# Kernel optimization log

Hardware: AMD Instinct MI355X
Metric: run time of the kernel (lower is better)

The kernel has to match this reference:

```python
import jax, jax.numpy as jnp
import numpy as np
from jax import lax

STRIDES = (8, 16, 32, 64, 128)
LEVEL_HW = ((100, 128), (50, 64), (25, 32), (13, 16), (7, 8))
NUM_CLASSES = 80
PRE_NMS_THRESH = 0.05
PRE_NMS_TOPK = 1000
NMS_THRESH = 0.6
MAX_DET = 100
CLS_OFFSET = 1.0e4  # > max image coordinate, separates classes for joint NMS


def setup_inputs() -> dict:
    key = jax.random.key(0)
    B = 16
    ks = jax.random.split(key, 3 * len(LEVEL_HW))
    inp = {}
    i = 0
    for lvl, (h, w) in enumerate(LEVEL_HW):
        # shift logits down so sigmoid scores are mostly below the 0.05 candidate
        # threshold (realistic detection sparsity)
        inp[f"logits_p{lvl + 3}"] = jax.random.normal(ks[i], (B, NUM_CLASSES, h, w), jnp.float32) - 4.0; i += 1
        inp[f"bbox_p{lvl + 3}"] = jax.random.uniform(ks[i], (B, 4, h, w), jnp.float32, minval=0.0, maxval=64.0); i += 1
        inp[f"ctr_p{lvl + 3}"] = jax.random.normal(ks[i], (B, 1, h, w), jnp.float32); i += 1
    inp["im_info"] = jnp.tile(jnp.array([[800.0, 1024.0]], jnp.float32), (B, 1))
    return inp


def _locations(h, w, stride):
    # FCOSLocation: center of each stride cell -> [HW, 2] as (x, y)
    sx = jnp.arange(w, dtype=jnp.float32) * stride + stride // 2
    sy = jnp.arange(h, dtype=jnp.float32) * stride + stride // 2
    yy, xx = jnp.meshgrid(sy, sx, indexing="ij")
    return jnp.stack([xx.reshape(-1), yy.reshape(-1)], axis=-1)


def _nms_single(boxes, scores, classes):
    # boxes [K,4], scores [K] (descending), classes [K] int
    off = classes.astype(jnp.float32)[:, None] * CLS_OFFSET
    nb = boxes + off  # class-offset trick -> per-class NMS in one pass
    areas = jnp.maximum(nb[:, 2] - nb[:, 0], 0.0) * jnp.maximum(nb[:, 3] - nb[:, 1], 0.0)

    def body(sc, _):
        i = jnp.argmax(sc)
        s = sc[i]
        bi = nb[i]
        xx1 = jnp.maximum(bi[0], nb[:, 0])
        yy1 = jnp.maximum(bi[1], nb[:, 1])
        xx2 = jnp.minimum(bi[2], nb[:, 2])
        yy2 = jnp.minimum(bi[3], nb[:, 3])
        inter = jnp.maximum(xx2 - xx1, 0.0) * jnp.maximum(yy2 - yy1, 0.0)
        iou = inter / (areas[i] + areas - inter + 1e-9)
        sc2 = jnp.where(iou >= NMS_THRESH, -jnp.inf, sc).at[i].set(-jnp.inf)
        return sc2, (i, s > 0.0)

    _, (idxs, valid) = lax.scan(body, scores, None, length=MAX_DET)
    det = jnp.concatenate(
        [boxes[idxs], scores[idxs][:, None], classes[idxs].astype(jnp.float32)[:, None]],
        axis=-1,
    )  # [MAX_DET, 6] = x1,y1,x2,y2,score,class
    return jnp.where(valid[:, None], det, 0.0)


def _forward(logits_p3, bbox_p3, ctr_p3, logits_p4, bbox_p4, ctr_p4,
             logits_p5, bbox_p5, ctr_p5, logits_p6, bbox_p6, ctr_p6,
             logits_p7, bbox_p7, ctr_p7, im_info):
    levels = [(logits_p3, bbox_p3, ctr_p3), (logits_p4, bbox_p4, ctr_p4),
              (logits_p5, bbox_p5, ctr_p5), (logits_p6, bbox_p6, ctr_p6),
              (logits_p7, bbox_p7, ctr_p7)]
    scores_l, boxes_l = [], []
    for (lg, rg, ct), stride in zip(levels, STRIDES):
        B, C, H, W = lg.shape
        cls = jax.nn.sigmoid(lg).transpose(0, 2, 3, 1).reshape(B, H * W, C)
        cen = jax.nn.sigmoid(ct).transpose(0, 2, 3, 1).reshape(B, H * W, 1)
        # candidate threshold on raw class prob, then modulate by centerness
        comb = jnp.where(cls > PRE_NMS_THRESH, cls * cen, 0.0)
        locs = _locations(H, W, stride)  # [HW, 2]
        reg = rg.transpose(0, 2, 3, 1).reshape(B, H * W, 4)  # (l, t, r, b)
        bx = jnp.stack([locs[None, :, 0] - reg[..., 0],
                        locs[None, :, 1] - reg[..., 1],
                        locs[None, :, 0] + reg[..., 2],
                        locs[None, :, 1] + reg[..., 3]], axis=-1)
        scores_l.append(comb)
        boxes_l.append(bx)
    scores = jnp.concatenate(scores_l, axis=1)  # [B, N, C]
    boxes = jnp.concatenate(boxes_l, axis=1)    # [B, N, 4]
    B, N, C = scores.shape
    vals, idx = lax.top_k(scores.reshape(B, N * C), PRE_NMS_TOPK)  # [B, K]
    loc = idx // C
    cls_id = idx % C
    cand = jnp.take_along_axis(boxes, loc[..., None], axis=1)  # [B, K, 4]
    h = im_info[:, 0:1]
    w = im_info[:, 1:2]
    x1 = jnp.clip(cand[..., 0], 0.0, w - 1.0)
    y1 = jnp.clip(cand[..., 1], 0.0, h - 1.0)
    x2 = jnp.clip(cand[..., 2], 0.0, w - 1.0)
    y2 = jnp.clip(cand[..., 3], 0.0, h - 1.0)
    cand = jnp.stack([x1, y1, x2, y2], axis=-1)
    sc = jnp.where(vals > 0.0, jnp.sqrt(jnp.maximum(vals, 0.0) + 1e-12), 0.0)
    return jax.vmap(_nms_single)(cand, sc, cls_id)  # [B, MAX_DET, 6]


def reference(logits_p3, bbox_p3, ctr_p3, logits_p4, bbox_p4, ctr_p4,
              logits_p5, bbox_p5, ctr_p5, logits_p6, bbox_p6, ctr_p6,
              logits_p7, bbox_p7, ctr_p7, im_info):
    return _forward(logits_p3, bbox_p3, ctr_p3, logits_p4, bbox_p4, ctr_p4,
                    logits_p5, bbox_p5, ctr_p5, logits_p6, bbox_p6, ctr_p6,
                    logits_p7, bbox_p7, ctr_p7, im_info)
```

## Files before the change

### kernel.cpp

```cpp
#include <hip/hip_runtime.h>
#include <math.h>

#pragma clang fp contract(off)

#define NB 16
#define NC 80
#define NTOT 17064
#define TOPK 1000
#define NBINS 8192
#define CAP 4096
#define MAXDET 100
#define CNTSTRIDE 64
#define CHUNK 128
#define GH 128
#define WSEGCAP 256
#define FB 16

struct Ptrs {
    const float* lg[5];
    const float* bb[5];
    const float* ct[5];
};

__device__ __forceinline__ void level_of(int n, int& l, int& hw, int& W,
                                         int& stride, int& half, int& HW) {
    if (n < 12800)      { l = 0; hw = n;         W = 128; stride = 8;   half = 4;  HW = 12800; }
    else if (n < 16000) { l = 1; hw = n - 12800; W = 64;  stride = 16;  half = 8;  HW = 3200;  }
    else if (n < 16800) { l = 2; hw = n - 16000; W = 32;  stride = 32;  half = 16; HW = 800;   }
    else if (n < 17008) { l = 3; hw = n - 16800; W = 16;  stride = 64;  half = 32; HW = 208;   }
    else                { l = 4; hw = n - 17008; W = 8;   stride = 128; half = 64; HW = 56;    }
}

__device__ __forceinline__ float fast_sig(float x) {
    float e = __expf(-x);
    return __builtin_amdgcn_rcpf(1.0f + e);
}

#define HG_EMIT(BITS, NN, CC, POS)                                            \
    {                                                                         \
        int lb = (int)(((BITS) - 32u) >> 19) - BINBASE;                       \
        lb = (lb < 0) ? 0 : ((lb > 63) ? 63 : lb);                            \
        atomicAdd(&whv[lb], 1u);             \
        unsigned pos_ = (POS);                                                \
        if (pos_ < WSEGCAP) {                                                 \
            unsigned idx_ = (unsigned)((NN) * NC + (CC));                     \
            segw[pos_] = ((unsigned long long)(BITS) << 32) | idx_;           \
        }                                                                     \
    }

#define LOADLG(I, V)                                                          \
    V = make_float4(-40.f, -40.f, -40.f, -40.f);                              \
    if ((I) < NF4) V = *(const float4*)(lgb + (size_t)(I) * 4);

#define QGATE(I, V, FM, K0, K1, K2, K3, HWQ, CCQ)                             \
    unsigned FM = 0, K0 = 0, K1 = 0, K2 = 0, K3 = 0;                          \
    int HWQ = 0, CCQ = 0;                                                     \
    if ((V).x > -2.47f || (V).y > -2.47f || (V).z > -2.47f || (V).w > -2.47f) { \
        CCQ = (I) / HW4; HWQ = (I) - CCQ * HW4;                               \
        float4 cv = *(const float4*)(ctb + HWQ * 4);                          \
        K0 = __float_as_uint(fast_sig((V).x) * fast_sig(cv.x));               \
        K1 = __float_as_uint(fast_sig((V).y) * fast_sig(cv.y));               \
        K2 = __float_as_uint(fast_sig((V).z) * fast_sig(cv.z));               \
        K3 = __float_as_uint(fast_sig((V).w) * fast_sig(cv.w));               \
        FM = (K0 >= FB_LO ? 1u : 0u) | (K1 >= FB_LO ? 2u : 0u)                \
           | (K2 >= FB_LO ? 4u : 0u) | (K3 >= FB_LO ? 8u : 0u);               \
    }

template<int HW4, int NF4, int LVOFF>
__device__ __forceinline__ void histg_level(const float* lgb, const float* ctb,
        int tid, int bx, int gx, unsigned FB_LO, int BINBASE, unsigned* whv,
        unsigned& wcnt, unsigned long long* segw, unsigned long long ltmask) {
    const int stride = gx * 512;
    int i0 = bx * 512;
    if (i0 >= NF4) return;
    float4 va, vb;
    LOADLG(i0 + tid, va)
    LOADLG(i0 + 256 + tid, vb)
    for (; i0 < NF4; ) {
        int in0 = i0 + stride;
        int ia = i0 + tid, ib = i0 + 256 + tid;
        float4 nva, nvb;
        LOADLG(in0 + tid, nva)
        LOADLG(in0 + 256 + tid, nvb)
        QGATE(ia, va, fmA, kA0, kA1, kA2, kA3, hwa, cca)
        QGATE(ib, vb, fmB, kB0, kB1, kB2, kB3, hwb, ccb)
        unsigned long long m0 = __ballot(fmA & 1u), m1 = __ballot(fmA & 2u);
        unsigned long long m2 = __ballot(fmA & 4u), m3 = __ballot(fmA & 8u);
        unsigned long long m4 = __ballot(fmB & 1u), m5 = __ballot(fmB & 2u);
        unsigned long long m6 = __ballot(fmB & 4u), m7 = __ballot(fmB & 8u);
        if (m0 | m1 | m2 | m3 | m4 | m5 | m6 | m7) {
            unsigned t0 = (unsigned)__popcll(m0), t1 = (unsigned)__popcll(m1);
            unsigned t2 = (unsigned)__popcll(m2), t3 = (unsigned)__popcll(m3);
            unsigned t4 = (unsigned)__popcll(m4), t5 = (unsigned)__popcll(m5);
            unsigned t6 = (unsigned)__popcll(m6), t7 = (unsigned)__popcll(m7);
            unsigned wb = wcnt;
            wcnt = wb + t0 + t1 + t2 + t3 + t4 + t5 + t6 + t7;
            int nb0a = LVOFF + hwa * 4, nb0b = LVOFF + hwb * 4;
            if (fmA & 1u) HG_EMIT(kA0, nb0a + 0, cca, wb + (unsigned)__popcll(m0 & ltmask))
            if (fmA & 2u) HG_EMIT(kA1, nb0a + 1, cca, wb + t0 + (unsigned)__popcll(m1 & ltmask))
            if (fmA & 4u) HG_EMIT(kA2, nb0a + 2, cca, wb + t0 + t1 + (unsigned)__popcll(m2 & ltmask))
            if (fmA & 8u) HG_EMIT(kA3, nb0a + 3, cca, wb + t0 + t1 + t2 + (unsigned)__popcll(m3 & ltmask))
            if (fmB & 1u) HG_EMIT(kB0, nb0b + 0, ccb, wb + t0 + t1 + t2 + t3 + (unsigned)__popcll(m4 & ltmask))
            if (fmB & 2u) HG_EMIT(kB1, nb0b + 1, ccb, wb + t0 + t1 + t2 + t3 + t4 + (unsigned)__popcll(m5 & ltmask))
            if (fmB & 4u) HG_EMIT(kB2, nb0b + 2, ccb, wb + t0 + t1 + t2 + t3 + t4 + t5 + (unsigned)__popcll(m6 & ltmask))
            if (fmB & 8u) HG_EMIT(kB3, nb0b + 3, ccb, wb + t0 + t1 + t2 + t3 + t4 + t5 + t6 + (unsigned)__popcll(m7 & ltmask))
        }
        i0 = in0;
        va = nva; vb = nvb;
    }
}
#undef LOADLG
#undef QGATE
#undef HG_EMIT

__global__ void __launch_bounds__(256) k_histB(Ptrs p, unsigned* hist, unsigned* cnt2,
                                               unsigned* wavecnt, unsigned long long* segs) {
    __shared__ unsigned wh[4][64];
    int b = blockIdx.y, tid = threadIdx.x, bx = blockIdx.x, gx = gridDim.x;
    int wv = tid >> 6, lane = tid & 63;
    if (bx == 0 && tid == 0) cnt2[(size_t)b * CNTSTRIDE] = 0;
    ((unsigned*)wh)[tid] = 0;
    unsigned FB_LO = __float_as_uint(0.08f) - 64u;
    int BINBASE = (int)(__float_as_uint(0.08f) >> 19);
    unsigned* whv = wh[wv];
    unsigned long long ltmask = (1ULL << lane) - 1ULL;
    unsigned wcnt = 0;
    unsigned long long* segw = segs + (((size_t)b * GH + bx) * 4 + wv) * WSEGCAP;

    histg_level<3200, 256000,     0>(p.lg[0] + (size_t)b * NC * 12800, p.ct[0] + (size_t)b * 12800, tid, bx, gx, FB_LO, BINBASE, whv, wcnt, segw, ltmask);
    histg_level< 800,  64000, 12800>(p.lg[1] + (size_t)b * NC * 3200,  p.ct[1] + (size_t)b * 3200,  tid, bx, gx, FB_LO, BINBASE, whv, wcnt, segw, ltmask);
    histg_level< 200,  16000, 16000>(p.lg[2] + (size_t)b * NC * 800,   p.ct[2] + (size_t)b * 800,   tid, bx, gx, FB_LO, BINBASE, whv, wcnt, segw, ltmask);
    histg_level<  52,   4160, 16800>(p.lg[3] + (size_t)b * NC * 208,   p.ct[3] + (size_t)b * 208,   tid, bx, gx, FB_LO, BINBASE, whv, wcnt, segw, ltmask);
    histg_level<  14,   1120, 17008>(p.lg[4] + (size_t)b * NC * 56,    p.ct[4] + (size_t)b * 56,    tid, bx, gx, FB_LO, BINBASE, whv, wcnt, segw, ltmask);

    if (lane == 0)
        wavecnt[((size_t)b * GH + bx) * 4 + wv] = wcnt;
    __syncthreads();
    if (tid < 64) {
        unsigned s = wh[0][tid] + wh[1][tid] + wh[2][tid] + wh[3][tid];
        hist[((size_t)b * GH + bx) * 64 + tid] = s;
    }
}

template<int HW4, int NF4>
__device__ __forceinline__ void histf_level(const float* lgb, const float* ctb,
                                            int tid, unsigned* hist) {
    for (int i0 = 0; i0 < NF4; i0 += 256) {
        int i = i0 + tid;
        if (i < NF4) {
            int c = i / HW4, hwf = i - c * HW4;
            float4 v = *(const float4*)(lgb + c * (HW4 * 4) + hwf * 4);
            if (v.x > -2.95f || v.y > -2.95f || v.z > -2.95f || v.w > -2.95f) {
                float4 cv = *(const float4*)(ctb + hwf * 4);
                float xs[4] = {v.x, v.y, v.z, v.w};
                float cs[4] = {cv.x, cv.y, cv.z, cv.w};
#pragma unroll
                for (int j = 0; j < 4; ++j) {
                    float x = xs[j];
                    if (x > -2.95f) {
                        float cls = fast_sig(x);
                        if (cls > 0.04999f) {
                            bool in = true;
                            if (cls < 0.05001f)
                                in = (1.0f / (1.0f + expf(-x))) > 0.05f;
                            if (in) {
                                float cen = fast_sig(cs[j]);
                                unsigned bits = __float_as_uint(cls * cen);
                                unsigned cb = (bits > 32u) ? bits - 32u : 0u;
                                atomicAdd(&hist[cb >> 19], 1u);
                            }
                        }
                    }
                }
            }
        }
    }
}

#define CD_J(J, X, CT, NB0, CC, F, K)                                         \
    if ((X) > xpre) {                                                         \
        float cls = 1.0f / (1.0f + expf(-(X)));                               \
        if (cls > 0.05f) {                                                    \
            float cen = 1.0f / (1.0f + expf(-(CT)));                          \
            float comb = cls * cen;                                           \
            unsigned bits = __float_as_uint(comb);                            \
            if ((bits >> 19) >= Tb) {                                         \
                unsigned idx = (unsigned)(((NB0) + (J)) * NC + (CC));         \
                K = ((unsigned long long)bits << 32) | (0xFFFFFFFFu - idx);   \
                F = true;                                                     \
            }                                                                 \
        }                                                                     \
    }

template<int HW4, int NF4, int LVOFF>
__device__ __forceinline__ void compact_level(const float* lgb, const float* ctb,
        int tid, int lane, int bx, int gx, unsigned Tb, float xpre,
        unsigned* cntb, unsigned long long* selb, unsigned long long ltmask) {
    for (int i0 = bx * 512; i0 < NF4; i0 += gx * 512) {
        int ia = i0 + tid, ib2 = i0 + 256 + tid;
        bool la = ia < NF4, lb2 = ib2 < NF4;
        float4 va = make_float4(-9.f, -9.f, -9.f, -9.f);
        float4 vb = make_float4(-9.f, -9.f, -9.f, -9.f);
        int hwa = 0, hwb = 0, cca = 0, ccb = 0;
        if (la) {
            cca = ia / HW4; hwa = ia - cca * HW4;
            va = *(const float4*)(lgb + cca * (HW4 * 4) + hwa * 4);
        }
        if (lb2) {
            ccb = ib2 / HW4; hwb = ib2 - ccb * HW4;
            vb = *(const float4*)(lgb + ccb * (HW4 * 4) + hwb * 4);
        }
        {
            bool f0 = false, f1 = false, f2 = false, f3 = false;
            unsigned long long k0 = 0, k1 = 0, k2 = 0, k3 = 0;
            if (va.x > xpre || va.y > xpre || va.z > xpre || va.w > xpre) {
                float4 cv = *(const float4*)(ctb + hwa * 4);
                int nb0 = LVOFF + hwa * 4;
                CD_J(0, va.x, cv.x, nb0, cca, f0, k0)
                CD_J(1, va.y, cv.y, nb0, cca, f1, k1)
                CD_J(2, va.z, cv.z, nb0, cca, f2, k2)
                CD_J(3, va.w, cv.w, nb0, cca, f3, k3)
            }
            unsigned long long m0 = __ballot(f0), m1 = __ballot(f1);
            unsigned long long m2 = __ballot(f2), m3 = __ballot(f3);
            if (m0 | m1 | m2 | m3) {
                unsigned t0 = (unsigned)__popcll(m0), t1 = (unsigned)__popcll(m1);
                unsigned t2 = (unsigned)__popcll(m2), t3 = (unsigned)__popcll(m3);
                int basep = 0;
                if (lane == 0) basep = (int)atomicAdd(cntb, t0 + t1 + t2 + t3);
                basep = __shfl(basep, 0);
                if (f0) { int pos = basep + (int)__popcll(m0 & ltmask);                       if (pos < CAP) selb[pos] = k0; }
                if (f1) { int pos = basep + (int)t0 + (int)__popcll(m1 & ltmask);             if (pos < CAP) selb[pos] = k1; }
                if (f2) { int pos = basep + (int)(t0 + t1) + (int)__popcll(m2 & ltmask);      if (pos < CAP) selb[pos] = k2; }
                if (f3) { int pos = basep + (int)(t0 + t1 + t2) + (int)__popcll(m3 & ltmask); if (pos < CAP) selb[pos] = k3; }
            }
        }
        {
            bool f0 = false, f1 = false, f2 = false, f3 = false;
            unsigned long long k0 = 0, k1 = 0, k2 = 0, k3 = 0;
            if (vb.x > xpre || vb.y > xpre || vb.z > xpre || vb.w > xpre) {
                float4 cv = *(const float4*)(ctb + hwb * 4);
                int nb0 = LVOFF + hwb * 4;
                CD_J(0, vb.x, cv.x, nb0, ccb, f0, k0)
                CD_J(1, vb.y, cv.y, nb0, ccb, f1, k1)
                CD_J(2, vb.z, cv.z, nb0, ccb, f2, k2)
                CD_J(3, vb.w, cv.w, nb0, ccb, f3, k3)
            }
            unsigned long long m0 = __ballot(f0), m1 = __ballot(f1);
            unsigned long long m2 = __ballot(f2), m3 = __ballot(f3);
            if (m0 | m1 | m2 | m3) {
                unsigned t0 = (unsigned)__popcll(m0), t1 = (unsigned)__popcll(m1);
                unsigned t2 = (unsigned)__popcll(m2), t3 = (unsigned)__popcll(m3);
                int basep = 0;
                if (lane == 0) basep = (int)atomicAdd(cntb, t0 + t1 + t2 + t3);
                basep = __shfl(basep, 0);
                if (f0) { int pos = basep + (int)__popcll(m0 & ltmask);                       if (pos < CAP) selb[pos] = k0; }
                if (f1) { int pos = basep + (int)t0 + (int)__popcll(m1 & ltmask);             if (pos < CAP) selb[pos] = k1; }
                if (f2) { int pos = basep + (int)(t0 + t1) + (int)__popcll(m2 & ltmask);      if (pos < CAP) selb[pos] = k2; }
                if (f3) { int pos = basep + (int)(t0 + t1 + t2) + (int)__popcll(m3 & ltmask); if (pos < CAP) selb[pos] = k3; }
            }
        }
    }
}
#undef CD_J

__device__ __forceinline__ void run_compact(const Ptrs& p, int b, int tid, int lane,
        int bx, int gx, unsigned Tb, unsigned* cnt2, unsigned long long* sel) {
    float mthr = __uint_as_float(Tb << 19);
    float xpre = -2.95f;
    if (mthr > 1e-37f && mthr < 1.0f) {
        float lm = logf(mthr / (1.0f - mthr)) - 0.01f;
        if (lm > xpre) xpre = lm;
    }
    unsigned long long ltmask = (1ULL << lane) - 1ULL;
    unsigned* cntb = cnt2 + (size_t)b * CNTSTRIDE;
    unsigned long long* selb = sel + (size_t)b * CAP;
    compact_level<3200, 256000,     0>(p.lg[0] + (size_t)b * NC * 12800, p.ct[0] + (size_t)b * 12800, tid, lane, bx, gx, Tb, xpre, cntb, selb, ltmask);
    compact_level< 800,  64000, 12800>(p.lg[1] + (size_t)b * NC * 3200,  p.ct[1] + (size_t)b * 3200,  tid, lane, bx, gx, Tb, xpre, cntb, selb, ltmask);
    compact_level< 200,  16000, 16000>(p.lg[2] + (size_t)b * NC * 800,   p.ct[2] + (size_t)b * 800,   tid, lane, bx, gx, Tb, xpre, cntb, selb, ltmask);
    compact_level<  52,   4160, 16800>(p.lg[3] + (size_t)b * NC * 208,   p.ct[3] + (size_t)b * 208,   tid, lane, bx, gx, Tb, xpre, cntb, selb, ltmask);
    compact_level<  14,   1120, 17008>(p.lg[4] + (size_t)b * NC * 56,    p.ct[4] + (size_t)b * 56,    tid, lane, bx, gx, Tb, xpre, cntb, selb, ltmask);
}

__global__ void __launch_bounds__(256) k_filter(Ptrs p, const unsigned* hist,
        const unsigned* wavecnt, const unsigned long long* segs,
        unsigned* cnt2, unsigned long long* sel) {
    __shared__ unsigned part[4][64];
    __shared__ unsigned red[64];
    __shared__ unsigned fullh[NBINS];
    __shared__ int s_T, s_ok;
    __shared__ unsigned s_ovf;
    int b = blockIdx.y, tid = threadIdx.x, bx = blockIdx.x;
    int bin = tid & 63, grp = tid >> 6, lane = tid & 63, wv = tid >> 6;
    int BINBASE = (int)(__float_as_uint(0.08f) >> 19);

    unsigned s = 0;
    for (int blk = grp; blk < GH; blk += 4)
        s += hist[((size_t)b * GH + blk) * 64 + bin];
    part[grp][bin] = s;
    if (tid == 0) s_ovf = 0;
    __syncthreads();
    if (tid < 64) red[tid] = part[0][tid] + part[1][tid] + part[2][tid] + part[3][tid];
    unsigned ov = 0;
    for (int i = tid; i < GH * 4; i += 256)
        ov |= (wavecnt[(size_t)b * GH * 4 + i] > WSEGCAP) ? 1u : 0u;
    if (ov) atomicOr(&s_ovf, 1u);
    __syncthreads();
    if (tid == 0) {
        unsigned suf1 = 0;
        for (int i = 1; i < 64; ++i) suf1 += red[i];
        unsigned run = 0; int Tl = 0;
        for (int i = 63; i >= 1; --i) {
            run += red[i];
            if (run >= TOPK) { Tl = i; break; }
        }
        s_ok = (suf1 >= TOPK);
        s_T = Tl + BINBASE;
    }
    __syncthreads();

    if (s_ok && !s_ovf) {
        unsigned Tb = (unsigned)s_T;
        unsigned FLO = (Tb << 19) - 64u;
        unsigned* cntb = cnt2 + (size_t)b * CNTSTRIDE;
        unsigned long long* selb = sel + (size_t)b * CAP;
        unsigned long long ltmask = (1ULL << lane) - 1ULL;
        for (int sg = bx * 4 + wv; sg < GH * 4; sg += FB * 4) {
            unsigned cs = wavecnt[(size_t)b * GH * 4 + sg];
            if (cs > WSEGCAP) cs = WSEGCAP;
            const unsigned long long* sp = segs + ((size_t)b * GH * 4 + sg) * WSEGCAP;
            for (unsigned e0 = 0; e0 < cs; e0 += 64) {
                unsigned e = e0 + (unsigned)lane;
                bool take = false;
                unsigned long long key = 0;
                if (e < cs) {
                    unsigned long long kk = sp[e];
                    if ((unsigned)(kk >> 32) >= FLO) {
                        unsigned idx = (unsigned)kk;
                        int n = (int)(idx / NC), c = (int)(idx - (unsigned)n * NC);
                        int l, hw, W, stride, half, HW;
                        level_of(n, l, hw, W, stride, half, HW);
                        float x   = p.lg[l][(size_t)b * NC * HW + (size_t)c * HW + hw];
                        float ctv = p.ct[l][(size_t)b * HW + hw];
                        float cls = 1.0f / (1.0f + expf(-x));
                        if (cls > 0.05f) {
                            float cen = 1.0f / (1.0f + expf(-ctv));
                            unsigned bits = __float_as_uint(cls * cen);
                            if ((bits >> 19) >= Tb) {
                                key = ((unsigned long long)bits << 32) | (0xFFFFFFFFu - idx);
                                take = true;
                            }
                        }
                    }
                }
                unsigned long long m = __ballot(take);
                if (m) {
                    unsigned tot = (unsigned)__popcll(m);
                    int basep = 0;
                    if (lane == 0) basep = (int)atomicAdd(cntb, tot);
                    basep = __shfl(basep, 0);
                    if (take) {
                        int pos = basep + (int)__popcll(m & ltmask);
                        if (pos < CAP) selb[pos] = key;
                    }
                }
            }
        }
        return;
    }

    if (!s_ok) {
        if (bx != 0) return;
        for (int i = tid; i < NBINS; i += 256) fullh[i] = 0;
        __syncthreads();
        histf_level<3200, 256000>(p.lg[0] + (size_t)b * NC * 12800, p.ct[0] + (size_t)b * 12800, tid, fullh);
        histf_level< 800,  64000>(p.lg[1] + (size_t)b * NC * 3200,  p.ct[1] + (size_t)b * 3200,  tid, fullh);
        histf_level< 200,  16000>(p.lg[2] + (size_t)b * NC * 800,   p.ct[2] + (size_t)b * 800,   tid, fullh);
        histf_level<  52,   4160>(p.lg[3] + (size_t)b * NC * 208,   p.ct[3] + (size_t)b * 208,   tid, fullh);
        histf_level<  14,   1120>(p.lg[4] + (size_t)b * NC * 56,    p.ct[4] + (size_t)b * 56,    tid, fullh);
        __syncthreads();
        if (tid == 0) {
            unsigned run = 0; int Tf = 0;
            for (int i = NBINS - 1; i >= 0; --i) {
                run += fullh[i];
                if (run >= TOPK) { Tf = i; break; }
            }
            s_T = Tf;
        }
        __syncthreads();
        run_compact(p, b, tid, lane, 0, 1, (unsigned)s_T, cnt2, sel);
        return;
    }

    run_compact(p, b, tid, lane, bx, FB, (unsigned)s_T, cnt2, sel);
}

__global__ void __launch_bounds__(256) k_rankdec(Ptrs p, const unsigned* cnt,
                                                 const unsigned long long* sel,
                                                 const float* im_info, float* cand) {
    __shared__ __align__(16) unsigned long long keys[CAP];
    int b = blockIdx.y, tid = threadIdx.x;
    unsigned M = cnt[(size_t)b * CNTSTRIDE];
    if (M > CAP) M = CAP;
    int s0 = blockIdx.x * 256;
    if (s0 >= (int)M) return;
    int Mpad = (int)((M + 1u) & ~1u);
    for (int i = tid; i < Mpad; i += 256)
        keys[i] = (i < (int)M) ? sel[(size_t)b * CAP + i] : 0ULL;
    __syncthreads();

    int s = s0 + tid;
    if (s >= (int)M) return;
    unsigned long long k = keys[s];
    int rank = 0;
    for (int j = 0; j < Mpad; j += 2) {
        ulonglong2 kk = *(const ulonglong2*)&keys[j];
        rank += (kk.x > k) ? 1 : 0;
        rank += (kk.y > k) ? 1 : 0;
    }
    if (rank >= TOPK) return;

    float Him = im_info[b * 2 + 0], Wim = im_info[b * 2 + 1];
    float xmax = Wim - 1.0f, ymax = Him - 1.0f;
    unsigned sb = (unsigned)(k >> 32);
    unsigned idx = 0xFFFFFFFFu - (unsigned)(k & 0xFFFFFFFFu);
    float val = __uint_as_float(sb);
    int n = idx / NC, c = idx - n * NC;
    int l, hw, W, stride, half, HW;
    level_of(n, l, hw, W, stride, half, HW);
    int wx = hw % W, hy = hw / W;
    float locx = (float)(wx * stride + half);
    float locy = (float)(hy * stride + half);
    const float* bb = p.bb[l] + (size_t)b * 4 * HW + hw;
    float r0 = bb[0], r1 = bb[(size_t)HW], r2 = bb[(size_t)2 * HW], r3 = bb[(size_t)3 * HW];
    float x1 = locx - r0, y1 = locy - r1, x2 = locx + r2, y2 = locy + r3;
    x1 = fminf(fmaxf(x1, 0.f), xmax);
    y1 = fminf(fmaxf(y1, 0.f), ymax);
    x2 = fminf(fmaxf(x2, 0.f), xmax);
    y2 = fminf(fmaxf(y2, 0.f), ymax);
    float scv = sqrtf(val + 1e-12f);
    float off = (float)c * 10000.0f;
    float a0 = x1 + off, a1 = y1 + off, a2 = x2 + off, a3 = y2 + off;
    float area = fmaxf(a2 - a0, 0.f) * fmaxf(a3 - a1, 0.f);
    float* dst = cand + ((size_t)b * TOPK + rank) * 12;
    *(float4*)(dst + 0) = make_float4(x1, y1, x2, y2);
    *(float4*)(dst + 4) = make_float4(a0, a1, a2, a3);
    *(float4*)(dst + 8) = make_float4(area, scv, (float)c, 0.f);
}

__global__ void __launch_bounds__(64) k_nms(const unsigned* cnt, const float* cand,
                                            float* out) {
    __shared__ float4 s_ob[CHUNK], s_nb[CHUNK], s_ms[CHUNK];
    int b = blockIdx.x, lane = threadIdx.x;
    unsigned M = cnt[(size_t)b * CNTSTRIDE];
    if (M > CAP) M = CAP;
    int ncand = (int)M < TOPK ? (int)M : TOPK;
    const float* src = cand + (size_t)b * TOPK * 12;
    float* ob = out + (size_t)b * MAXDET * 6;

    int na = 0;
    float4 a0b = make_float4(0.f, 0.f, 0.f, 0.f);
    float4 a1b = make_float4(0.f, 0.f, 0.f, 0.f);
    float a0a = 0.f, a1a = 0.f;

    for (int base = 0; base < ncand && na < MAXDET; base += CHUNK) {
        int cn = ncand - base; if (cn > CHUNK) cn = CHUNK;
        for (int cidx = lane; cidx < cn; cidx += 64) {
            const float* s = src + (size_t)(base + cidx) * 12;
            s_ob[cidx] = *(const float4*)(s + 0);
            s_nb[cidx] = *(const float4*)(s + 4);
            s_ms[cidx] = *(const float4*)(s + 8);
        }
        __syncthreads();
        for (int r = 0; r < cn && na < MAXDET; ++r) {
            float4 cb = s_nb[r];
            float ca = s_ms[r].x;
            bool sup = false;
            if (lane < na) {
                float xx1 = fmaxf(a0b.x, cb.x);
                float yy1 = fmaxf(a0b.y, cb.y);
                float xx2 = fminf(a0b.z, cb.z);
                float yy2 = fminf(a0b.w, cb.w);
                float inter = fmaxf(xx2 - xx1, 0.f) * fmaxf(yy2 - yy1, 0.f);
                float iou = inter / (((a0a + ca) - inter) + 1e-9f);
                sup = (iou >= 0.6f);
            }
            if (lane + 64 < na) {
                float xx1 = fmaxf(a1b.x, cb.x);
                float yy1 = fmaxf(a1b.y, cb.y);
                float xx2 = fminf(a1b.z, cb.z);
                float yy2 = fminf(a1b.w, cb.w);
                float inter = fmaxf(xx2 - xx1, 0.f) * fmaxf(yy2 - yy1, 0.f);
                float iou = inter / (((a1a + ca) - inter) + 1e-9f);
                sup |= (iou >= 0.6f);
            }
            if (__ballot(sup) == 0ULL) {
                if (lane == (na & 63)) {
                    if (na < 64) { a0b = cb; a0a = ca; }
                    else         { a1b = cb; a1a = ca; }
                }
                if (lane == 0) {
                    float4 o4 = s_ob[r]; float4 m4 = s_ms[r];
                    ob[na * 6 + 0] = o4.x; ob[na * 6 + 1] = o4.y;
                    ob[na * 6 + 2] = o4.z; ob[na * 6 + 3] = o4.w;
                    ob[na * 6 + 4] = m4.y; ob[na * 6 + 5] = m4.z;
                }
                ++na;
            }
        }
        __syncthreads();
    }
    for (int q = na * 6 + lane; q < MAXDET * 6; q += 64)
        ob[q] = 0.f;
}

extern "C" void kernel_launch(void* const* d_in, const int* in_sizes, int n_in,
                              void* d_out, int out_size, void* d_ws, size_t ws_size,
                              hipStream_t stream) {
    Ptrs p;
    for (int l = 0; l < 5; ++l) {
        p.lg[l] = (const float*)d_in[3 * l + 0];
        p.bb[l] = (const float*)d_in[3 * l + 1];
        p.ct[l] = (const float*)d_in[3 * l + 2];
    }
    const float* im_info = (const float*)d_in[15];
    float* out = (float*)d_out;
    unsigned char* w = (unsigned char*)d_ws;

    unsigned* hist           = (unsigned*)(w);
    unsigned* cnt2           = (unsigned*)(w + 524288);
    unsigned* wavecnt        = (unsigned*)(w + 528384);
    unsigned long long* segs = (unsigned long long*)(w + 561152);
    unsigned long long* sel  = (unsigned long long*)(w + 17338368);
    float* cand              = (float*)(w + 17862656);

    k_histB<<<dim3(GH, NB), 256, 0, stream>>>(p, hist, cnt2, wavecnt, segs);
    k_filter<<<dim3(FB, NB), 256, 0, stream>>>(p, hist, wavecnt, segs, cnt2, sel);
    k_rankdec<<<dim3(16, NB), 256, 0, stream>>>(p, cnt2, sel, im_info, cand);
    k_nms<<<NB, 64, 0, stream>>>(cnt2, cand, out);
}
```

Baseline: 234.8 us.

## Split histogram pass into pure logit sweep plus separate gating kernel

The fused histogram kernel is split in two. A streaming sweep only thresholds raw logits and compacts survivors (raw value plus level-encoded index) per wave. A new small-grid gate kernel then loads centerness, computes the sigmoid product, builds the histogram and writes the filtered segments. The aim is to keep the bandwidth-bound sweep lean by taking the scattered centerness loads, transcendental math and shared-memory atomics off its critical path. The cost is an extra kernel launch, an extra round trip of survivors through global memory, and a larger workspace with new overflow caps.

```diff
diff --git a/kernel.cpp b/kernel.cpp
--- a/kernel.cpp
+++ b/kernel.cpp
@@ -13,7 +13,9 @@
 #define CNTSTRIDE 64
 #define CHUNK 128
 #define GH 128
-#define WSEGCAP 256
+#define ACAP 512
+#define HB 16
+#define BSEGCAP 2048
 #define FB 16
 
 struct Ptrs {
@@ -36,40 +38,22 @@
     return __builtin_amdgcn_rcpf(1.0f + e);
 }
 
-#define HG_EMIT(BITS, NN, CC, POS)                                            \
-    {                                                                         \
-        int lb = (int)(((BITS) - 32u) >> 19) - BINBASE;                       \
-        lb = (lb < 0) ? 0 : ((lb > 63) ? 63 : lb);                            \
-        atomicAdd(&whv[lb], 1u);             \
-        unsigned pos_ = (POS);                                                \
-        if (pos_ < WSEGCAP) {                                                 \
-            unsigned idx_ = (unsigned)((NN) * NC + (CC));                     \
-            segw[pos_] = ((unsigned long long)(BITS) << 32) | idx_;           \
-        }                                                                     \
-    }
-
 #define LOADLG(I, V)                                                          \
     V = make_float4(-40.f, -40.f, -40.f, -40.f);                              \
     if ((I) < NF4) V = *(const float4*)(lgb + (size_t)(I) * 4);
 
-#define QGATE(I, V, FM, K0, K1, K2, K3, HWQ, CCQ)                             \
-    unsigned FM = 0, K0 = 0, K1 = 0, K2 = 0, K3 = 0;                          \
-    int HWQ = 0, CCQ = 0;                                                     \
-    if ((V).x > -2.47f || (V).y > -2.47f || (V).z > -2.47f || (V).w > -2.47f) { \
-        CCQ = (I) / HW4; HWQ = (I) - CCQ * HW4;                               \
-        float4 cv = *(const float4*)(ctb + HWQ * 4);                          \
-        K0 = __float_as_uint(fast_sig((V).x) * fast_sig(cv.x));               \
-        K1 = __float_as_uint(fast_sig((V).y) * fast_sig(cv.y));               \
-        K2 = __float_as_uint(fast_sig((V).z) * fast_sig(cv.z));               \
-        K3 = __float_as_uint(fast_sig((V).w) * fast_sig(cv.w));               \
-        FM = (K0 >= FB_LO ? 1u : 0u) | (K1 >= FB_LO ? 2u : 0u)                \
-           | (K2 >= FB_LO ? 4u : 0u) | (K3 >= FB_LO ? 8u : 0u);               \
-    }
-
-template<int HW4, int NF4, int LVOFF>
-__device__ __forceinline__ void histg_level(const float* lgb, const float* ctb,
-        int tid, int bx, int gx, unsigned FB_LO, int BINBASE, unsigned* whv,
-        unsigned& wcnt, unsigned long long* segw, unsigned long long ltmask) {
+#define SW_EMIT(X, ENC, POS)                                                  \
+    {                                                                         \
+        unsigned pos_ = (POS);                                                \
+        if (pos_ < ACAP)                                                      \
+            survw[pos_] = ((unsigned long long)__float_as_uint(X) << 32)      \
+                        | (ENC);                                              \
+    }
+
+template<int NF4>
+__device__ __forceinline__ void sweepA(const float* lgb, unsigned lvl,
+        int tid, int bx, int gx, unsigned& wcnt,
+        unsigned long long* survw, unsigned long long ltmask) {
     const int stride = gx * 512;
     int i0 = bx * 512;
     if (i0 >= NF4) return;
@@ -82,12 +66,14 @@
         float4 nva, nvb;
         LOADLG(in0 + tid, nva)
         LOADLG(in0 + 256 + tid, nvb)
-        QGATE(ia, va, fmA, kA0, kA1, kA2, kA3, hwa, cca)
-        QGATE(ib, vb, fmB, kB0, kB1, kB2, kB3, hwb, ccb)
-        unsigned long long m0 = __ballot(fmA & 1u), m1 = __ballot(fmA & 2u);
-        unsigned long long m2 = __ballot(fmA & 4u), m3 = __ballot(fmA & 8u);
-        unsigned long long m4 = __ballot(fmB & 1u), m5 = __ballot(fmB & 2u);
-        unsigned long long m6 = __ballot(fmB & 4u), m7 = __ballot(fmB & 8u);
+        bool f0 = va.x > -2.47f, f1 = va.y > -2.47f;
+        bool f2 = va.z > -2.47f, f3 = va.w > -2.47f;
+        bool f4 = vb.x > -2.47f, f5 = vb.y > -2.47f;
+        bool f6 = vb.z > -2.47f, f7 = vb.w > -2.47f;
+        unsigned long long m0 = __ballot(f0), m1 = __ballot(f1);
+        unsigned long long m2 = __ballot(f2), m3 = __ballot(f3);
+        unsigned long long m4 = __ballot(f4), m5 = __ballot(f5);
+        unsigned long long m6 = __ballot(f6), m7 = __ballot(f7);
         if (m0 | m1 | m2 | m3 | m4 | m5 | m6 | m7) {
             unsigned t0 = (unsigned)__popcll(m0), t1 = (unsigned)__popcll(m1);
             unsigned t2 = (unsigned)__popcll(m2), t3 = (unsigned)__popcll(m3);
@@ -95,50 +81,110 @@
             unsigned t6 = (unsigned)__popcll(m6), t7 = (unsigned)__popcll(m7);
             unsigned wb = wcnt;
             wcnt = wb + t0 + t1 + t2 + t3 + t4 + t5 + t6 + t7;
-            int nb0a = LVOFF + hwa * 4, nb0b = LVOFF + hwb * 4;
-            if (fmA & 1u) HG_EMIT(kA0, nb0a + 0, cca, wb + (unsigned)__popcll(m0 & ltmask))
-            if (fmA & 2u) HG_EMIT(kA1, nb0a + 1, cca, wb + t0 + (unsigned)__popcll(m1 & ltmask))
-            if (fmA & 4u) HG_EMIT(kA2, nb0a + 2, cca, wb + t0 + t1 + (unsigned)__popcll(m2 & ltmask))
-            if (fmA & 8u) HG_EMIT(kA3, nb0a + 3, cca, wb + t0 + t1 + t2 + (unsigned)__popcll(m3 & ltmask))
-            if (fmB & 1u) HG_EMIT(kB0, nb0b + 0, ccb, wb + t0 + t1 + t2 + t3 + (unsigned)__popcll(m4 & ltmask))
-            if (fmB & 2u) HG_EMIT(kB1, nb0b + 1, ccb, wb + t0 + t1 + t2 + t3 + t4 + (unsigned)__popcll(m5 & ltmask))
-            if (fmB & 4u) HG_EMIT(kB2, nb0b + 2, ccb, wb + t0 + t1 + t2 + t3 + t4 + t5 + (unsigned)__popcll(m6 & ltmask))
-            if (fmB & 8u) HG_EMIT(kB3, nb0b + 3, ccb, wb + t0 + t1 + t2 + t3 + t4 + t5 + t6 + (unsigned)__popcll(m7 & ltmask))
+            unsigned ea = ((unsigned)ia << 2) | (lvl << 24);
+            unsigned eb = ((unsigned)ib << 2) | (lvl << 24);
+            if (f0) SW_EMIT(va.x, ea + 0u, wb + (unsigned)__popcll(m0 & ltmask))
+            if (f1) SW_EMIT(va.y, ea + 1u, wb + t0 + (unsigned)__popcll(m1 & ltmask))
+            if (f2) SW_EMIT(va.z, ea + 2u, wb + t0 + t1 + (unsigned)__popcll(m2 & ltmask))
+            if (f3) SW_EMIT(va.w, ea + 3u, wb + t0 + t1 + t2 + (unsigned)__popcll(m3 & ltmask))
+            if (f4) SW_EMIT(vb.x, eb + 0u, wb + t0 + t1 + t2 + t3 + (unsigned)__popcll(m4 & ltmask))
+            if (f5) SW_EMIT(vb.y, eb + 1u, wb + t0 + t1 + t2 + t3 + t4 + (unsigned)__popcll(m5 & ltmask))
+            if (f6) SW_EMIT(vb.z, eb + 2u, wb + t0 + t1 + t2 + t3 + t4 + t5 + (unsigned)__popcll(m6 & ltmask))
+            if (f7) SW_EMIT(vb.w, eb + 3u, wb + t0 + t1 + t2 + t3 + t4 + t5 + t6 + (unsigned)__popcll(m7 & ltmask))
         }
         i0 = in0;
         va = nva; vb = nvb;
     }
 }
 #undef LOADLG
-#undef QGATE
-#undef HG_EMIT
-
-__global__ void __launch_bounds__(256) k_histB(Ptrs p, unsigned* hist, unsigned* cnt2,
-                                               unsigned* wavecnt, unsigned long long* segs) {
-    __shared__ unsigned wh[4][64];
+#undef SW_EMIT
+
+__global__ void __launch_bounds__(256) k_sweep(Ptrs p, unsigned* cnt2,
+        unsigned* survwcnt, unsigned long long* surv) {
     int b = blockIdx.y, tid = threadIdx.x, bx = blockIdx.x, gx = gridDim.x;
     int wv = tid >> 6, lane = tid & 63;
     if (bx == 0 && tid == 0) cnt2[(size_t)b * CNTSTRIDE] = 0;
+    unsigned long long ltmask = (1ULL << lane) - 1ULL;
+    unsigned wcnt = 0;
+    unsigned long long* survw = surv + (((size_t)b * GH + bx) * 4 + wv) * ACAP;
+
+    sweepA<256000>(p.lg[0] + (size_t)b * NC * 12800, 0u, tid, bx, gx, wcnt, survw, ltmask);
+    sweepA< 64000>(p.lg[1] + (size_t)b * NC * 3200,  1u, tid, bx, gx, wcnt, survw, ltmask);
+    sweepA< 16000>(p.lg[2] + (size_t)b * NC * 800,   2u, tid, bx, gx, wcnt, survw, ltmask);
+    sweepA<  4160>(p.lg[3] + (size_t)b * NC * 208,   3u, tid, bx, gx, wcnt, survw, ltmask);
+    sweepA<  1120>(p.lg[4] + (size_t)b * NC * 56,    4u, tid, bx, gx, wcnt, survw, ltmask);
+
+    if (lane == 0)
+        survwcnt[((size_t)b * GH + bx) * 4 + wv] = wcnt;
+}
+
+__global__ void __launch_bounds__(256) k_gate(Ptrs p, const unsigned* survwcnt,
+        const unsigned long long* surv, unsigned* hist, unsigned* wavecnt,
+        unsigned long long* segs) {
+    __shared__ unsigned wh[4][64];
+    int b = blockIdx.y, tid = threadIdx.x, bx = blockIdx.x;
+    int wv = tid >> 6, lane = tid & 63;
     ((unsigned*)wh)[tid] = 0;
     unsigned FB_LO = __float_as_uint(0.08f) - 64u;
     int BINBASE = (int)(__float_as_uint(0.08f) >> 19);
     unsigned* whv = wh[wv];
     unsigned long long ltmask = (1ULL << lane) - 1ULL;
     unsigned wcnt = 0;
-    unsigned long long* segw = segs + (((size_t)b * GH + bx) * 4 + wv) * WSEGCAP;
-
-    histg_level<3200, 256000,     0>(p.lg[0] + (size_t)b * NC * 12800, p.ct[0] + (size_t)b * 12800, tid, bx, gx, FB_LO, BINBASE, whv, wcnt, segw, ltmask);
-    histg_level< 800,  64000, 12800>(p.lg[1] + (size_t)b * NC * 3200,  p.ct[1] + (size_t)b * 3200,  tid, bx, gx, FB_LO, BINBASE, whv, wcnt, segw, ltmask);
-    histg_level< 200,  16000, 16000>(p.lg[2] + (size_t)b * NC * 800,   p.ct[2] + (size_t)b * 800,   tid, bx, gx, FB_LO, BINBASE, whv, wcnt, segw, ltmask);
-    histg_level<  52,   4160, 16800>(p.lg[3] + (size_t)b * NC * 208,   p.ct[3] + (size_t)b * 208,   tid, bx, gx, FB_LO, BINBASE, whv, wcnt, segw, ltmask);
-    histg_level<  14,   1120, 17008>(p.lg[4] + (size_t)b * NC * 56,    p.ct[4] + (size_t)b * 56,    tid, bx, gx, FB_LO, BINBASE, whv, wcnt, segw, ltmask);
-
+    unsigned long long* segw = segs + (((size_t)b * HB + bx) * 4 + wv) * BSEGCAP;
+
+    for (int sg = bx * 4 + wv; sg < GH * 4; sg += HB * 4) {
+        unsigned cs = survwcnt[(size_t)b * GH * 4 + sg];
+        if (cs > ACAP) cs = ACAP;
+        const unsigned long long* sp = surv + ((size_t)b * GH * 4 + sg) * ACAP;
+        for (unsigned e0 = 0; e0 < cs; e0 += 64) {
+            unsigned e = e0 + (unsigned)lane;
+            bool take = false;
+            unsigned bits = 0, idx = 0;
+            if (e < cs) {
+                unsigned long long kk = sp[e];
+                float x = __uint_as_float((unsigned)(kk >> 32));
+                unsigned enc = (unsigned)kk;
+                int lvl = (int)(enc >> 24);
+                int e4 = (int)(enc & 0x00FFFFFFu);
+                int HW, NOFF;
+                const float* ctb;
+                if (lvl == 0)      { HW = 12800; NOFF = 0;     ctb = p.ct[0]; }
+                else if (lvl == 1) { HW = 3200;  NOFF = 12800; ctb = p.ct[1]; }
+                else if (lvl == 2) { HW = 800;   NOFF = 16000; ctb = p.ct[2]; }
+                else if (lvl == 3) { HW = 208;   NOFF = 16800; ctb = p.ct[3]; }
+                else               { HW = 56;    NOFF = 17008; ctb = p.ct[4]; }
+                int cc = e4 / HW;
+                int hwl = e4 - cc * HW;
+                float ctv = ctb[(size_t)b * HW + hwl];
+                unsigned b2 = __float_as_uint(fast_sig(x) * fast_sig(ctv));
+                if (b2 >= FB_LO) {
+                    int lb = (int)((b2 - 32u) >> 19) - BINBASE;
+                    lb = (lb < 0) ? 0 : ((lb > 63) ? 63 : lb);
+                    atomicAdd(&whv[lb], 1u);
+                    bits = b2;
+                    idx = (unsigned)((NOFF + hwl) * NC + cc);
+                    take = true;
+                }
+            }
+            unsigned long long m = __ballot(take);
+            if (m) {
+                unsigned tot = (unsigned)__popcll(m);
+                unsigned wb = wcnt;
+                wcnt = wb + tot;
+                if (take) {
+                    unsigned pos = wb + (unsigned)__popcll(m & ltmask);
+                    if (pos < BSEGCAP)
+                        segw[pos] = ((unsigned long long)bits << 32) | idx;
+                }
+            }
+        }
+    }
     if (lane == 0)
-        wavecnt[((size_t)b * GH + bx) * 4 + wv] = wcnt;
+        wavecnt[((size_t)b * HB + bx) * 4 + wv] = wcnt;
     __syncthreads();
     if (tid < 64) {
         unsigned s = wh[0][tid] + wh[1][tid] + wh[2][tid] + wh[3][tid];
-        hist[((size_t)b * GH + bx) * 64 + tid] = s;
+        hist[((size_t)b * HB + bx) * 64 + tid] = s;
     }
 }
 
@@ -283,8 +329,8 @@
 }
 
 __global__ void __launch_bounds__(256) k_filter(Ptrs p, const unsigned* hist,
-        const unsigned* wavecnt, const unsigned long long* segs,
-        unsigned* cnt2, unsigned long long* sel) {
+        const unsigned* survwcnt, const unsigned* wavecnt,
+        const unsigned long long* segs, unsigned* cnt2, unsigned long long* sel) {
     __shared__ unsigned part[4][64];
     __shared__ unsigned red[64];
     __shared__ unsigned fullh[NBINS];
@@ -295,15 +341,17 @@
     int BINBASE = (int)(__float_as_uint(0.08f) >> 19);
 
     unsigned s = 0;
-    for (int blk = grp; blk < GH; blk += 4)
-        s += hist[((size_t)b * GH + blk) * 64 + bin];
+    for (int blk = grp; blk < HB; blk += 4)
+        s += hist[((size_t)b * HB + blk) * 64 + bin];
     part[grp][bin] = s;
     if (tid == 0) s_ovf = 0;
     __syncthreads();
     if (tid < 64) red[tid] = part[0][tid] + part[1][tid] + part[2][tid] + part[3][tid];
     unsigned ov = 0;
     for (int i = tid; i < GH * 4; i += 256)
-        ov |= (wavecnt[(size_t)b * GH * 4 + i] > WSEGCAP) ? 1u : 0u;
+        ov |= (survwcnt[(size_t)b * GH * 4 + i] > ACAP) ? 1u : 0u;
+    for (int i = tid; i < HB * 4; i += 256)
+        ov |= (wavecnt[(size_t)b * HB * 4 + i] > BSEGCAP) ? 1u : 0u;
     if (ov) atomicOr(&s_ovf, 1u);
     __syncthreads();
     if (tid == 0) {
@@ -325,10 +373,10 @@
         unsigned* cntb = cnt2 + (size_t)b * CNTSTRIDE;
         unsigned long long* selb = sel + (size_t)b * CAP;
         unsigned long long ltmask = (1ULL << lane) - 1ULL;
-        for (int sg = bx * 4 + wv; sg < GH * 4; sg += FB * 4) {
-            unsigned cs = wavecnt[(size_t)b * GH * 4 + sg];
-            if (cs > WSEGCAP) cs = WSEGCAP;
-            const unsigned long long* sp = segs + ((size_t)b * GH * 4 + sg) * WSEGCAP;
+        for (int sg = bx * 4 + wv; sg < HB * 4; sg += FB * 4) {
+            unsigned cs = wavecnt[(size_t)b * HB * 4 + sg];
+            if (cs > BSEGCAP) cs = BSEGCAP;
+            const unsigned long long* sp = segs + ((size_t)b * HB * 4 + sg) * BSEGCAP;
             for (unsigned e0 = 0; e0 < cs; e0 += 64) {
                 unsigned e = e0 + (unsigned)lane;
                 bool take = false;
@@ -528,14 +576,17 @@
     unsigned char* w = (unsigned char*)d_ws;
 
     unsigned* hist           = (unsigned*)(w);
-    unsigned* cnt2           = (unsigned*)(w + 524288);
-    unsigned* wavecnt        = (unsigned*)(w + 528384);
-    unsigned long long* segs = (unsigned long long*)(w + 561152);
-    unsigned long long* sel  = (unsigned long long*)(w + 17338368);
-    float* cand              = (float*)(w + 17862656);
-
-    k_histB<<<dim3(GH, NB), 256, 0, stream>>>(p, hist, cnt2, wavecnt, segs);
-    k_filter<<<dim3(FB, NB), 256, 0, stream>>>(p, hist, wavecnt, segs, cnt2, sel);
+    unsigned* cnt2           = (unsigned*)(w + 65536);
+    unsigned* survwcnt       = (unsigned*)(w + 69632);
+    unsigned* wavecnt        = (unsigned*)(w + 102400);
+    unsigned long long* surv = (unsigned long long*)(w + 106496);
+    unsigned long long* segs = (unsigned long long*)(w + 33660928);
+    unsigned long long* sel  = (unsigned long long*)(w + 50438144);
+    float* cand              = (float*)(w + 50962432);
+
+    k_sweep<<<dim3(GH, NB), 256, 0, stream>>>(p, cnt2, survwcnt, surv);
+    k_gate<<<dim3(HB, NB), 256, 0, stream>>>(p, survwcnt, surv, hist, wavecnt, segs);
+    k_filter<<<dim3(FB, NB), 256, 0, stream>>>(p, hist, survwcnt, wavecnt, segs, cnt2, sel);
     k_rankdec<<<dim3(16, NB), 256, 0, stream>>>(p, cnt2, sel, im_info, cand);
     k_nms<<<NB, 64, 0, stream>>>(cnt2, cand, out);
 }
```

Result: slower. 240.9 us (+2.6%).
